# Kernel tuning notes

Hardware: AMD Instinct MI355X
Metric: run time of the kernel (lower is better)

Reference implementation:

```python
import jax, jax.numpy as jnp
import numpy as np

B, D, NT, NZ = 16384, 64, 128, 2048


def setup_inputs() -> dict:
    key = jax.random.key(0)
    ks = jax.random.split(key, 5)
    return {
        "t": jax.random.uniform(ks[0], (1,), dtype=jnp.float32),
        "z": jax.random.normal(ks[1], (B, D), dtype=jnp.float32),
        "logp_z": jnp.zeros((B, 1), jnp.float32),
        "centres_z": jax.random.normal(ks[2], (NZ, D), dtype=jnp.float32),
        "log_sigmas_z": jnp.zeros((NZ,), jnp.float32),
        "centres_t": jax.random.normal(ks[3], (NT, 1), dtype=jnp.float32),
        "log_sigmas_t": jnp.zeros((NT,), jnp.float32),
        "W": 0.01 * jax.random.normal(ks[4], (D, NT, NZ + 1), dtype=jnp.float32),
    }


def _gauss(r):
    return jnp.exp(-r * r)


def _forward(t, z, centres_z, log_sigmas_z, centres_t, log_sigmas_t, W):
    # time RBF features Phi_t: (NT,)
    r_t = jnp.abs(t.reshape(1, 1) - centres_t.reshape(1, -1)) / jnp.exp(log_sigmas_t)
    phi_t = _gauss(r_t).reshape(-1)
    W_t = jnp.einsum('dij,i->dj', W, phi_t)  # (D, NZ+1)
    Wz, bias = W_t[:, :-1], W_t[:, -1]       # bias comes from the appended ones column
    # z RBF features via squared-distance identity (avoids [B,NZ,D] blowup)
    sq = (jnp.sum(z * z, axis=1, keepdims=True)
          + jnp.sum(centres_z * centres_z, axis=1)[None, :]
          - 2.0 * z @ centres_z.T)
    sq = jnp.maximum(sq, 0.0)                 # (B, NZ) squared distances
    inv_s2 = jnp.exp(-2.0 * log_sigmas_z)     # 1/sigma_j^2, (NZ,)
    phi_z = jnp.exp(-sq * inv_s2)             # gaussian(||z-c_j||/s_j), (B, NZ)
    dz_dt = phi_z @ Wz.T + bias               # (B, D)
    # exact Jacobian trace for gaussian basis:
    #   d phi_j / d z_i = -2 * phi_j * (z_i - c_{j,i}) / s_j^2
    #   tr(J)_b = sum_j phi_{b,j} * inv_s2_j * (-2) * (sum_i Wz[i,j] z_{b,i} - sum_i Wz[i,j] c_{j,i})
    q = jnp.einsum('dj,jd->j', Wz, centres_z)  # (NZ,)
    trace = -2.0 * jnp.sum(phi_z * inv_s2 * (z @ Wz - q), axis=1)  # (B,)
    dlogp_z_dt = -trace[:, None]               # (B, 1)
    return dz_dt, dlogp_z_dt


def reference(t, z, logp_z, centres_z, log_sigmas_z, centres_t, log_sigmas_t, W):
    return _forward(t, z, centres_z, log_sigmas_z, centres_t, log_sigmas_t, W)
```

## Files before the change

kernel.cpp:

```cpp
#include <hip/hip_runtime.h>
#include <math.h>

typedef unsigned int uint;
typedef unsigned short ushort;
typedef unsigned char uchar;
typedef unsigned long ulong_;
typedef __attribute__((ext_vector_type(4))) float f32x4;

#define BB  16384
#define DD  64
#define NT_ 128
#define NZ_ 2048
#define NJ_ 2049

#define BIAS_OFF 0
#define IL2_OFF  64
#define A0_OFF   2112
#define NIQ_OFF  4160
#define CZ8A_OFF 6208
#define CZ8B_OFF 22592
#define WZ8A_OFF 38976
#define WZ8B_OFF 55360
#define WZBP_OFF 71744
#define PART_OFF 104512

#if __has_builtin(__builtin_amdgcn_cvt_pk_fp8_f32)
__device__ __forceinline__ uint pk4_fp8(float a, float b, float c, float d) {
  int v = __builtin_amdgcn_cvt_pk_fp8_f32(a, b, 0, false);
  v = __builtin_amdgcn_cvt_pk_fp8_f32(c, d, v, true);
  return (uint)v;
}
__device__ __forceinline__ uchar f8_1(float x) {
  return (uchar)(__builtin_amdgcn_cvt_pk_fp8_f32(x, x, 0, false) & 0xFF);
}
#else
__device__ __forceinline__ uint sw_f8(float x) {
  uint u = __float_as_uint(x);
  uint s = (u >> 24) & 0x80u;
  float ax = __uint_as_float(u & 0x7FFFFFFFu);
  if (!(ax >= 0.015625f)) return s;
  if (ax >= 448.f) return s | 0x7Eu;
  uint q = __float_as_uint(ax);
  q += 0x7FFFFu + ((q >> 20) & 1u);
  uint e = (q >> 23) - 120u;
  return s | ((e & 0xFu) << 3) | ((q >> 20) & 7u);
}
__device__ __forceinline__ uchar f8_1(float x) { return (uchar)sw_f8(x); }
__device__ __forceinline__ uint pk4_fp8(float a, float b, float c, float d) {
  return sw_f8(a) | (sw_f8(b) << 8) | (sw_f8(c) << 16) | (sw_f8(d) << 24);
}
#endif

__global__ __launch_bounds__(256) void k_wt1(
    const float* __restrict__ t, const float* __restrict__ ct,
    const float* __restrict__ lst, const float* __restrict__ W,
    float* __restrict__ part)
{
  __shared__ float ph[32];
  int tx = threadIdx.x;
  int d  = blockIdx.y;
  int ic = blockIdx.z;
  if (tx < 32) {
    int i = ic * 32 + tx;
    float r = fabsf(t[0] - ct[i]) * __expf(-lst[i]);
    ph[tx] = __expf(-r * r);
  }
  __syncthreads();
  int j = blockIdx.x * 256 + tx;
  if (j >= NJ_) return;
  const float* Wp = W + (size_t)d * NT_ * NJ_ + (size_t)(ic * 32) * NJ_ + j;
  float acc = 0.f;
#pragma unroll
  for (int k = 0; k < 32; ++k) acc += Wp[(size_t)k * NJ_] * ph[k];
  part[((size_t)ic * 64 + d) * NJ_ + j] = acc;
}

__global__ __launch_bounds__(256) void k_prep2(
    const float* __restrict__ part, const float* __restrict__ cz,
    const float* __restrict__ lsz,
    float* __restrict__ bias,
    float* __restrict__ il2a, float* __restrict__ a0a, float* __restrict__ niqa,
    uchar* __restrict__ cz8a, uchar* __restrict__ cz8b,
    uchar* __restrict__ wz8a, uchar* __restrict__ wz8b,
    uchar* __restrict__ wzbp8)
{
  __shared__ float wt[64][9];
  int tid = threadIdx.x;
  int cb0 = blockIdx.x * 8;
#pragma unroll
  for (int h = 0; h < 2; ++h) {
    int f = h * 256 + tid;
    int d = f >> 3, c = f & 7;
    size_t idx = (size_t)d * NJ_ + cb0 + c;
    float s = part[idx] + part[(size_t)64 * NJ_ + idx]
            + part[(size_t)128 * NJ_ + idx] + part[(size_t)192 * NJ_ + idx];
    wt[d][c] = s;
    int cg = cb0 + c;
    wzbp8[((size_t)(cg >> 5) * 64 + d) * 32 + (cg & 31)] = f8_1(s);
  }
  if (blockIdx.x == 0 && tid < 64) {
    size_t idx = (size_t)tid * NJ_ + 2048;
    bias[tid] = part[idx] + part[(size_t)64 * NJ_ + idx]
              + part[(size_t)128 * NJ_ + idx] + part[(size_t)192 * NJ_ + idx];
  }
  __syncthreads();
  int cl = tid >> 5;
  int k  = tid & 31;
  int c  = cb0 + cl;
  float cv0 = cz[(size_t)c * DD + k];
  float cv1 = cz[(size_t)c * DD + 32 + k];
  cz8a[(size_t)c * 32 + k] = f8_1(cv0);
  cz8b[(size_t)c * 32 + k] = f8_1(cv1);
  float w0 = wt[k][cl], w1 = wt[32 + k][cl];
  wz8a[(size_t)c * 32 + k] = f8_1(w0);
  wz8b[(size_t)c * 32 + k] = f8_1(w1);
  float ca = cv0 * cv0 + cv1 * cv1;
  float qa = w0 * cv0 + w1 * cv1;
  qa += __shfl_xor(qa, 1);  ca += __shfl_xor(ca, 1);
  qa += __shfl_xor(qa, 2);  ca += __shfl_xor(ca, 2);
  qa += __shfl_xor(qa, 4);  ca += __shfl_xor(ca, 4);
  qa += __shfl_xor(qa, 8);  ca += __shfl_xor(ca, 8);
  qa += __shfl_xor(qa, 16); ca += __shfl_xor(ca, 16);
  if (k == 0) {
    float inv = __expf(-2.f * lsz[c]);
    float il2 = inv * 1.44269504f;
    il2a[c] = il2;
    a0a[c]  = -ca * il2;
    niqa[c] = -inv * qa;
  }
}

__global__ __launch_bounds__(256, 2) void k_fused(
    const float* __restrict__ z,
    const uchar* __restrict__ cz8a, const uchar* __restrict__ cz8b,
    const uchar* __restrict__ wz8a, const uchar* __restrict__ wz8b,
    const uchar* __restrict__ wzbp8,
    const float* __restrict__ il2a, const float* __restrict__ a0a,
    const float* __restrict__ niqa,
    const float* __restrict__ bias, float* __restrict__ out)
{
  __shared__ float eps[32 * 68];
  __shared__ float dlr[4][32];

  int tid  = threadIdx.x;
  int ws   = tid >> 6;
  int lane = tid & 63;
  int lrow = lane & 15, quad = lane >> 4;
  int b0 = blockIdx.x * 32;

  long az[2][2];
  float nzz[2];
#pragma unroll
  for (int mt = 0; mt < 2; ++mt) {
    const float* zr = z + (size_t)(b0 + mt * 16 + lrow) * DD + quad * 8;
    float4 v0 = *(const float4*)zr;
    float4 v1 = *(const float4*)(zr + 4);
    float4 v2 = *(const float4*)(zr + 32);
    float4 v3 = *(const float4*)(zr + 36);
    uint l0 = pk4_fp8(v0.x, v0.y, v0.z, v0.w);
    uint l1 = pk4_fp8(v1.x, v1.y, v1.z, v1.w);
    uint h0 = pk4_fp8(v2.x, v2.y, v2.z, v2.w);
    uint h1 = pk4_fp8(v3.x, v3.y, v3.z, v3.w);
    az[mt][0] = (long)(((ulong_)l1 << 32) | l0);
    az[mt][1] = (long)(((ulong_)h1 << 32) | h0);
    float ss = v0.x * v0.x + v0.y * v0.y + v0.z * v0.z + v0.w * v0.w
             + v1.x * v1.x + v1.y * v1.y + v1.z * v1.z + v1.w * v1.w
             + v2.x * v2.x + v2.y * v2.y + v2.z * v2.z + v2.w * v2.w
             + v3.x * v3.x + v3.y * v3.y + v3.z * v3.z + v3.w * v3.w;
    ss += __shfl_xor(ss, 16);
    ss += __shfl_xor(ss, 32);
    nzz[mt] = -ss;
  }

  f32x4 acc[2][4];
#pragma unroll
  for (int mt = 0; mt < 2; ++mt)
#pragma unroll
    for (int nt = 0; nt < 4; ++nt) acc[mt][nt] = (f32x4){0.f, 0.f, 0.f, 0.f};
  float dl[2] = {0.f, 0.f};

  const f32x4 zero = (f32x4){0.f, 0.f, 0.f, 0.f};
  int cbase = ws * 512;

  long Abc0[2][2], Abc1[2][2], Abw0[2][2], Abw1[2][2], Abb[2][4];
#define LOADB(PAR, C0)                                                         \
  do {                                                                         \
    int c0_ = (C0);                                                            \
    _Pragma("unroll")                                                          \
    for (int nt = 0; nt < 2; ++nt) {                                           \
      int cg_ = c0_ + nt * 16 + lrow;                                          \
      size_t ro_ = (size_t)cg_ * 32 + quad * 8;                                \
      Abc0[PAR][nt] = *(const long*)(cz8a + ro_);                              \
      Abc1[PAR][nt] = *(const long*)(cz8b + ro_);                              \
      Abw0[PAR][nt] = *(const long*)(wz8a + ro_);                              \
      Abw1[PAR][nt] = *(const long*)(wz8b + ro_);                              \
    }                                                                          \
    size_t cb_ = (size_t)(c0_ >> 5) * 64 * 32;                                 \
    _Pragma("unroll")                                                          \
    for (int nt = 0; nt < 4; ++nt)                                             \
      Abb[PAR][nt] =                                                           \
          *(const long*)(wzbp8 + cb_ + (size_t)(nt * 16 + lrow) * 32 + quad * 8); \
  } while (0)

  LOADB(0, cbase);
#pragma unroll 2
  for (int it = 0; it < 16; ++it) {
    int par = it & 1;
    int c0  = cbase + it * 32;

    float4 ilv[2], a0v[2], nqv[2];
#pragma unroll
    for (int nt = 0; nt < 2; ++nt) {
      int cb = c0 + nt * 16 + quad * 4;
      ilv[nt] = *(const float4*)&il2a[cb];
      a0v[nt] = *(const float4*)&a0a[cb];
      nqv[nt] = *(const float4*)&niqa[cb];
    }

    f32x4 d1a[2][2], d2a[2][2];
#pragma unroll
    for (int nt = 0; nt < 2; ++nt)
#pragma unroll
      for (int mt = 0; mt < 2; ++mt) {
        f32x4 d1 = __builtin_amdgcn_mfma_f32_16x16x32_fp8_fp8(Abc0[par][nt], az[mt][0], zero, 0, 0, 0);
        d1       = __builtin_amdgcn_mfma_f32_16x16x32_fp8_fp8(Abc1[par][nt], az[mt][1], d1,   0, 0, 0);
        f32x4 d2 = __builtin_amdgcn_mfma_f32_16x16x32_fp8_fp8(Abw0[par][nt], az[mt][0], zero, 0, 0, 0);
        d2       = __builtin_amdgcn_mfma_f32_16x16x32_fp8_fp8(Abw1[par][nt], az[mt][1], d2,   0, 0, 0);
        d1a[nt][mt] = d1;
        d2a[nt][mt] = d2;
      }

    LOADB(par ^ 1, cbase + ((it + 1) & 15) * 32);

    uint u00, u01, u10, u11;
#pragma unroll
    for (int mt = 0; mt < 2; ++mt)
#pragma unroll
      for (int nt = 0; nt < 2; ++nt) {
        float pv[4];
#pragma unroll
        for (int i = 0; i < 4; ++i) {
          float il2 = ilv[nt][i];
          float t2  = d1a[nt][mt][i] + d1a[nt][mt][i];
          float uu  = fmaf(il2, nzz[mt], a0v[nt][i]);
          float e   = fmaf(t2, il2, uu);
          e = fminf(e, 0.f);
          float p;
          asm("v_exp_f32 %0, %1" : "=v"(p) : "v"(e));
          float g = fmaf(d2a[nt][mt][i] * 0.69314718f, il2, nqv[nt][i]);
          dl[mt] = fmaf(p, g, dl[mt]);
          pv[i] = p;
        }
        uint uv = pk4_fp8(pv[0], pv[1], pv[2], pv[3]);
        if (mt == 0) { if (nt == 0) u00 = uv; else u01 = uv; }
        else         { if (nt == 0) u10 = uv; else u11 = uv; }
      }

    int  sl = lrow + ((lane & 16) << 1);
    bool hh = lane >= 32;
    uint l0a = __shfl(u00, sl),      l1a = __shfl(u01, sl);
    uint h0a = __shfl(u00, sl + 16), h1a = __shfl(u01, sl + 16);
    uint lo0 = hh ? l1a : l0a,       hi0 = hh ? h1a : h0a;
    long ap0 = (long)(((ulong_)hi0 << 32) | lo0);
    uint l0b = __shfl(u10, sl),      l1b = __shfl(u11, sl);
    uint h0b = __shfl(u10, sl + 16), h1b = __shfl(u11, sl + 16);
    uint lo1 = hh ? l1b : l0b,       hi1 = hh ? h1b : h0b;
    long ap1 = (long)(((ulong_)hi1 << 32) | lo1);

    __builtin_amdgcn_s_setprio(1);
#pragma unroll
    for (int nt = 0; nt < 4; ++nt) {
      acc[0][nt] = __builtin_amdgcn_mfma_f32_16x16x32_fp8_fp8(ap0, Abb[par][nt], acc[0][nt], 0, 0, 0);
      acc[1][nt] = __builtin_amdgcn_mfma_f32_16x16x32_fp8_fp8(ap1, Abb[par][nt], acc[1][nt], 0, 0, 0);
    }
    __builtin_amdgcn_s_setprio(0);
  }
#undef LOADB

#pragma unroll
  for (int mt = 0; mt < 2; ++mt) {
    float v = dl[mt];
    v += __shfl_xor(v, 16);
    v += __shfl_xor(v, 32);
    if (quad == 0) dlr[ws][mt * 16 + lrow] = v;
  }

  for (int s = 0; s < 4; ++s) {
    __syncthreads();
    if (ws == s) {
#pragma unroll
      for (int mt = 0; mt < 2; ++mt)
#pragma unroll
        for (int nt = 0; nt < 4; ++nt)
#pragma unroll
          for (int i = 0; i < 4; ++i) {
            int r = mt * 16 + quad * 4 + i;
            int d = nt * 16 + lrow;
            if (s == 0) eps[r * 68 + d] = acc[mt][nt][i];
            else        eps[r * 68 + d] += acc[mt][nt][i];
          }
    }
  }
  __syncthreads();

  {
    int r = tid >> 3, d0 = (tid & 7) * 8;
    float4 e0 = *(const float4*)&eps[r * 68 + d0];
    float4 e1 = *(const float4*)&eps[r * 68 + d0 + 4];
    float4 bv0 = *(const float4*)&bias[d0];
    float4 bv1 = *(const float4*)&bias[d0 + 4];
    float4 o0, o1;
    o0.x = e0.x + bv0.x; o0.y = e0.y + bv0.y; o0.z = e0.z + bv0.z; o0.w = e0.w + bv0.w;
    o1.x = e1.x + bv1.x; o1.y = e1.y + bv1.y; o1.z = e1.z + bv1.z; o1.w = e1.w + bv1.w;
    *(float4*)&out[(size_t)(b0 + r) * DD + d0]     = o0;
    *(float4*)&out[(size_t)(b0 + r) * DD + d0 + 4] = o1;
  }
  if (tid < 32) {
    float s = dlr[0][tid] + dlr[1][tid] + dlr[2][tid] + dlr[3][tid];
    out[(size_t)BB * DD + b0 + tid] = 2.f * s;
  }
}

extern "C" void kernel_launch(void* const* d_in, const int* in_sizes, int n_in,
                              void* d_out, int out_size, void* d_ws, size_t ws_size,
                              hipStream_t stream)
{
  const float* t   = (const float*)d_in[0];
  const float* z   = (const float*)d_in[1];
  const float* cz  = (const float*)d_in[3];
  const float* lsz = (const float*)d_in[4];
  const float* ct  = (const float*)d_in[5];
  const float* lst = (const float*)d_in[6];
  const float* W   = (const float*)d_in[7];
  float* out = (float*)d_out;
  float* ws  = (float*)d_ws;

  float*  bias = ws + BIAS_OFF;
  float*  il2a = ws + IL2_OFF;
  float*  a0a  = ws + A0_OFF;
  float*  niqa = ws + NIQ_OFF;
  uchar*  cz8a = (uchar*)(ws + CZ8A_OFF);
  uchar*  cz8b = (uchar*)(ws + CZ8B_OFF);
  uchar*  wz8a = (uchar*)(ws + WZ8A_OFF);
  uchar*  wz8b = (uchar*)(ws + WZ8B_OFF);
  uchar*  wzbp8 = (uchar*)(ws + WZBP_OFF);
  float*  part = ws + PART_OFF;

  k_wt1<<<dim3(9, 64, 4), 256, 0, stream>>>(t, ct, lst, W, part);
  k_prep2<<<dim3(256), 256, 0, stream>>>(part, cz, lsz, bias,
                                         il2a, a0a, niqa,
                                         cz8a, cz8b, wz8a, wz8b, wzbp8);
  k_fused<<<dim3(BB / 32), 256, 0, stream>>>(z, cz8a, cz8b,
                                             wz8a, wz8b, wzbp8,
                                             il2a, a0a, niqa, bias, out);
}
```

Baseline: 137.5 us.

## Shrink fused kernel row tile to 16 and drop register double-buffering

The fused kernel now handles 16 batch rows per block instead of 32, doubling the grid. It also removes the software-pipelined double-buffered B-operand loads in favour of plain per-iteration loads with no unrolling, and drops the launch-bounds occupancy hint. This lowers register pressure and raises parallelism. The cost is that every centre/weight fragment is loaded twice as often per batch row, which halves operand reuse, and load latency is no longer hidden by prefetch.

```diff
diff --git a/kernel.cpp b/kernel.cpp
--- a/kernel.cpp
+++ b/kernel.cpp
@@ -130,7 +130,7 @@
   }
 }
 
-__global__ __launch_bounds__(256, 2) void k_fused(
+__global__ __launch_bounds__(256) void k_fused(
     const float* __restrict__ z,
     const uchar* __restrict__ cz8a, const uchar* __restrict__ cz8b,
     const uchar* __restrict__ wz8a, const uchar* __restrict__ wz8b,
@@ -139,20 +139,19 @@
     const float* __restrict__ niqa,
     const float* __restrict__ bias, float* __restrict__ out)
 {
-  __shared__ float eps[32 * 68];
-  __shared__ float dlr[4][32];
+  __shared__ float eps[16 * 68];
+  __shared__ float dlr[4][16];
 
   int tid  = threadIdx.x;
   int ws   = tid >> 6;
   int lane = tid & 63;
   int lrow = lane & 15, quad = lane >> 4;
-  int b0 = blockIdx.x * 32;
-
-  long az[2][2];
-  float nzz[2];
-#pragma unroll
-  for (int mt = 0; mt < 2; ++mt) {
-    const float* zr = z + (size_t)(b0 + mt * 16 + lrow) * DD + quad * 8;
+  int b0 = blockIdx.x * 16;
+
+  long az[2];
+  float nzz;
+  {
+    const float* zr = z + (size_t)(b0 + lrow) * DD + quad * 8;
     float4 v0 = *(const float4*)zr;
     float4 v1 = *(const float4*)(zr + 4);
     float4 v2 = *(const float4*)(zr + 32);
@@ -161,161 +160,129 @@
     uint l1 = pk4_fp8(v1.x, v1.y, v1.z, v1.w);
     uint h0 = pk4_fp8(v2.x, v2.y, v2.z, v2.w);
     uint h1 = pk4_fp8(v3.x, v3.y, v3.z, v3.w);
-    az[mt][0] = (long)(((ulong_)l1 << 32) | l0);
-    az[mt][1] = (long)(((ulong_)h1 << 32) | h0);
+    az[0] = (long)(((ulong_)l1 << 32) | l0);
+    az[1] = (long)(((ulong_)h1 << 32) | h0);
     float ss = v0.x * v0.x + v0.y * v0.y + v0.z * v0.z + v0.w * v0.w
              + v1.x * v1.x + v1.y * v1.y + v1.z * v1.z + v1.w * v1.w
              + v2.x * v2.x + v2.y * v2.y + v2.z * v2.z + v2.w * v2.w
              + v3.x * v3.x + v3.y * v3.y + v3.z * v3.z + v3.w * v3.w;
     ss += __shfl_xor(ss, 16);
     ss += __shfl_xor(ss, 32);
-    nzz[mt] = -ss;
-  }
-
-  f32x4 acc[2][4];
-#pragma unroll
-  for (int mt = 0; mt < 2; ++mt)
-#pragma unroll
-    for (int nt = 0; nt < 4; ++nt) acc[mt][nt] = (f32x4){0.f, 0.f, 0.f, 0.f};
-  float dl[2] = {0.f, 0.f};
+    nzz = -ss;
+  }
+
+  f32x4 acc[4];
+#pragma unroll
+  for (int nt = 0; nt < 4; ++nt) acc[nt] = (f32x4){0.f, 0.f, 0.f, 0.f};
+  float dl = 0.f;
 
   const f32x4 zero = (f32x4){0.f, 0.f, 0.f, 0.f};
   int cbase = ws * 512;
 
-  long Abc0[2][2], Abc1[2][2], Abw0[2][2], Abw1[2][2], Abb[2][4];
-#define LOADB(PAR, C0)                                                         \
-  do {                                                                         \
-    int c0_ = (C0);                                                            \
-    _Pragma("unroll")                                                          \
-    for (int nt = 0; nt < 2; ++nt) {                                           \
-      int cg_ = c0_ + nt * 16 + lrow;                                          \
-      size_t ro_ = (size_t)cg_ * 32 + quad * 8;                                \
-      Abc0[PAR][nt] = *(const long*)(cz8a + ro_);                              \
-      Abc1[PAR][nt] = *(const long*)(cz8b + ro_);                              \
-      Abw0[PAR][nt] = *(const long*)(wz8a + ro_);                              \
-      Abw1[PAR][nt] = *(const long*)(wz8b + ro_);                              \
-    }                                                                          \
-    size_t cb_ = (size_t)(c0_ >> 5) * 64 * 32;                                 \
-    _Pragma("unroll")                                                          \
-    for (int nt = 0; nt < 4; ++nt)                                             \
-      Abb[PAR][nt] =                                                           \
-          *(const long*)(wzbp8 + cb_ + (size_t)(nt * 16 + lrow) * 32 + quad * 8); \
-  } while (0)
-
-  LOADB(0, cbase);
-#pragma unroll 2
+#pragma unroll 1
   for (int it = 0; it < 16; ++it) {
-    int par = it & 1;
-    int c0  = cbase + it * 32;
-
+    int c0 = cbase + it * 32;
+
+    long Abc0[2], Abc1[2], Abw0[2], Abw1[2], Abb[4];
     float4 ilv[2], a0v[2], nqv[2];
 #pragma unroll
     for (int nt = 0; nt < 2; ++nt) {
+      int cg = c0 + nt * 16 + lrow;
+      size_t ro = (size_t)cg * 32 + quad * 8;
+      Abc0[nt] = *(const long*)(cz8a + ro);
+      Abc1[nt] = *(const long*)(cz8b + ro);
+      Abw0[nt] = *(const long*)(wz8a + ro);
+      Abw1[nt] = *(const long*)(wz8b + ro);
       int cb = c0 + nt * 16 + quad * 4;
       ilv[nt] = *(const float4*)&il2a[cb];
       a0v[nt] = *(const float4*)&a0a[cb];
       nqv[nt] = *(const float4*)&niqa[cb];
     }
-
-    f32x4 d1a[2][2], d2a[2][2];
-#pragma unroll
-    for (int nt = 0; nt < 2; ++nt)
-#pragma unroll
-      for (int mt = 0; mt < 2; ++mt) {
-        f32x4 d1 = __builtin_amdgcn_mfma_f32_16x16x32_fp8_fp8(Abc0[par][nt], az[mt][0], zero, 0, 0, 0);
-        d1       = __builtin_amdgcn_mfma_f32_16x16x32_fp8_fp8(Abc1[par][nt], az[mt][1], d1,   0, 0, 0);
-        f32x4 d2 = __builtin_amdgcn_mfma_f32_16x16x32_fp8_fp8(Abw0[par][nt], az[mt][0], zero, 0, 0, 0);
-        d2       = __builtin_amdgcn_mfma_f32_16x16x32_fp8_fp8(Abw1[par][nt], az[mt][1], d2,   0, 0, 0);
-        d1a[nt][mt] = d1;
-        d2a[nt][mt] = d2;
+    {
+      size_t cb_ = (size_t)(c0 >> 5) * 64 * 32;
+#pragma unroll
+      for (int nt = 0; nt < 4; ++nt)
+        Abb[nt] = *(const long*)(wzbp8 + cb_ + (size_t)(nt * 16 + lrow) * 32 + quad * 8);
+    }
+
+    f32x4 d1a[2], d2a[2];
+#pragma unroll
+    for (int nt = 0; nt < 2; ++nt) {
+      f32x4 d1 = __builtin_amdgcn_mfma_f32_16x16x32_fp8_fp8(Abc0[nt], az[0], zero, 0, 0, 0);
+      d1       = __builtin_amdgcn_mfma_f32_16x16x32_fp8_fp8(Abc1[nt], az[1], d1,   0, 0, 0);
+      f32x4 d2 = __builtin_amdgcn_mfma_f32_16x16x32_fp8_fp8(Abw0[nt], az[0], zero, 0, 0, 0);
+      d2       = __builtin_amdgcn_mfma_f32_16x16x32_fp8_fp8(Abw1[nt], az[1], d2,   0, 0, 0);
+      d1a[nt] = d1;
+      d2a[nt] = d2;
+    }
+
+    uint u0, u1;
+#pragma unroll
+    for (int nt = 0; nt < 2; ++nt) {
+      float pv[4];
+#pragma unroll
+      for (int i = 0; i < 4; ++i) {
+        float il2 = ilv[nt][i];
+        float t2  = d1a[nt][i] + d1a[nt][i];
+        float uu  = fmaf(il2, nzz, a0v[nt][i]);
+        float e   = fmaf(t2, il2, uu);
+        e = fminf(e, 0.f);
+        float p;
+        asm("v_exp_f32 %0, %1" : "=v"(p) : "v"(e));
+        float g = fmaf(d2a[nt][i] * 0.69314718f, il2, nqv[nt][i]);
+        dl = fmaf(p, g, dl);
+        pv[i] = p;
       }
-
-    LOADB(par ^ 1, cbase + ((it + 1) & 15) * 32);
-
-    uint u00, u01, u10, u11;
-#pragma unroll
-    for (int mt = 0; mt < 2; ++mt)
-#pragma unroll
-      for (int nt = 0; nt < 2; ++nt) {
-        float pv[4];
-#pragma unroll
-        for (int i = 0; i < 4; ++i) {
-          float il2 = ilv[nt][i];
-          float t2  = d1a[nt][mt][i] + d1a[nt][mt][i];
-          float uu  = fmaf(il2, nzz[mt], a0v[nt][i]);
-          float e   = fmaf(t2, il2, uu);
-          e = fminf(e, 0.f);
-          float p;
-          asm("v_exp_f32 %0, %1" : "=v"(p) : "v"(e));
-          float g = fmaf(d2a[nt][mt][i] * 0.69314718f, il2, nqv[nt][i]);
-          dl[mt] = fmaf(p, g, dl[mt]);
-          pv[i] = p;
-        }
-        uint uv = pk4_fp8(pv[0], pv[1], pv[2], pv[3]);
-        if (mt == 0) { if (nt == 0) u00 = uv; else u01 = uv; }
-        else         { if (nt == 0) u10 = uv; else u11 = uv; }
-      }
+      uint uv = pk4_fp8(pv[0], pv[1], pv[2], pv[3]);
+      if (nt == 0) u0 = uv; else u1 = uv;
+    }
 
     int  sl = lrow + ((lane & 16) << 1);
     bool hh = lane >= 32;
-    uint l0a = __shfl(u00, sl),      l1a = __shfl(u01, sl);
-    uint h0a = __shfl(u00, sl + 16), h1a = __shfl(u01, sl + 16);
-    uint lo0 = hh ? l1a : l0a,       hi0 = hh ? h1a : h0a;
+    uint l0a = __shfl(u0, sl),      l1a = __shfl(u1, sl);
+    uint h0a = __shfl(u0, sl + 16), h1a = __shfl(u1, sl + 16);
+    uint lo0 = hh ? l1a : l0a,      hi0 = hh ? h1a : h0a;
     long ap0 = (long)(((ulong_)hi0 << 32) | lo0);
-    uint l0b = __shfl(u10, sl),      l1b = __shfl(u11, sl);
-    uint h0b = __shfl(u10, sl + 16), h1b = __shfl(u11, sl + 16);
-    uint lo1 = hh ? l1b : l0b,       hi1 = hh ? h1b : h0b;
-    long ap1 = (long)(((ulong_)hi1 << 32) | lo1);
 
     __builtin_amdgcn_s_setprio(1);
 #pragma unroll
-    for (int nt = 0; nt < 4; ++nt) {
-      acc[0][nt] = __builtin_amdgcn_mfma_f32_16x16x32_fp8_fp8(ap0, Abb[par][nt], acc[0][nt], 0, 0, 0);
-      acc[1][nt] = __builtin_amdgcn_mfma_f32_16x16x32_fp8_fp8(ap1, Abb[par][nt], acc[1][nt], 0, 0, 0);
-    }
+    for (int nt = 0; nt < 4; ++nt)
+      acc[nt] = __builtin_amdgcn_mfma_f32_16x16x32_fp8_fp8(ap0, Abb[nt], acc[nt], 0, 0, 0);
     __builtin_amdgcn_s_setprio(0);
   }
-#undef LOADB
-
-#pragma unroll
-  for (int mt = 0; mt < 2; ++mt) {
-    float v = dl[mt];
+
+  {
+    float v = dl;
     v += __shfl_xor(v, 16);
     v += __shfl_xor(v, 32);
-    if (quad == 0) dlr[ws][mt * 16 + lrow] = v;
+    if (quad == 0) dlr[ws][lrow] = v;
   }
 
   for (int s = 0; s < 4; ++s) {
     __syncthreads();
     if (ws == s) {
 #pragma unroll
-      for (int mt = 0; mt < 2; ++mt)
-#pragma unroll
-        for (int nt = 0; nt < 4; ++nt)
-#pragma unroll
-          for (int i = 0; i < 4; ++i) {
-            int r = mt * 16 + quad * 4 + i;
-            int d = nt * 16 + lrow;
-            if (s == 0) eps[r * 68 + d] = acc[mt][nt][i];
-            else        eps[r * 68 + d] += acc[mt][nt][i];
-          }
+      for (int nt = 0; nt < 4; ++nt)
+#pragma unroll
+        for (int i = 0; i < 4; ++i) {
+          int r = quad * 4 + i;
+          int d = nt * 16 + lrow;
+          if (s == 0) eps[r * 68 + d] = acc[nt][i];
+          else        eps[r * 68 + d] += acc[nt][i];
+        }
     }
   }
   __syncthreads();
 
   {
-    int r = tid >> 3, d0 = (tid & 7) * 8;
+    int r = tid >> 4, d0 = (tid & 15) * 4;
     float4 e0 = *(const float4*)&eps[r * 68 + d0];
-    float4 e1 = *(const float4*)&eps[r * 68 + d0 + 4];
     float4 bv0 = *(const float4*)&bias[d0];
-    float4 bv1 = *(const float4*)&bias[d0 + 4];
-    float4 o0, o1;
+    float4 o0;
     o0.x = e0.x + bv0.x; o0.y = e0.y + bv0.y; o0.z = e0.z + bv0.z; o0.w = e0.w + bv0.w;
-    o1.x = e1.x + bv1.x; o1.y = e1.y + bv1.y; o1.z = e1.z + bv1.z; o1.w = e1.w + bv1.w;
-    *(float4*)&out[(size_t)(b0 + r) * DD + d0]     = o0;
-    *(float4*)&out[(size_t)(b0 + r) * DD + d0 + 4] = o1;
-  }
-  if (tid < 32) {
+    *(float4*)&out[(size_t)(b0 + r) * DD + d0] = o0;
+  }
+  if (tid < 16) {
     float s = dlr[0][tid] + dlr[1][tid] + dlr[2][tid] + dlr[3][tid];
     out[(size_t)BB * DD + b0 + tid] = 2.f * s;
   }
@@ -350,7 +317,7 @@
   k_prep2<<<dim3(256), 256, 0, stream>>>(part, cz, lsz, bias,
                                          il2a, a0a, niqa,
                                          cz8a, cz8b, wz8a, wz8b, wzbp8);
-  k_fused<<<dim3(BB / 32), 256, 0, stream>>>(z, cz8a, cz8b,
+  k_fused<<<dim3(BB / 16), 256, 0, stream>>>(z, cz8a, cz8b,
                                              wz8a, wz8b, wzbp8,
                                              il2a, a0a, niqa, bias, out);
 }
```

Measured after the change: 153.0 us. +11.2%, slower.

## Stage per-tile B operands into LDS via global_load_lds double buffering

Applied to the files above, without the earlier changes.

Replaces the per-lane register prefetch of fp8 centre/weight tiles and per-centre constants with asynchronous global-to-LDS loads into a per-wave double buffer, waited on with vmcnt. Each iteration reads its operands from LDS, which cuts register pressure and the scattered small global loads. It also precomputes inv sigma^2 so the exponent and trace terms need fewer FMAs. The cost is more LDS use per block (about 57KB), which may limit occupancy. Correctness relies on the manual waitcnt ordering, since there is no barrier between the async LDS writes and the reads.

```diff
diff --git a/kernel.cpp b/kernel.cpp
--- a/kernel.cpp
+++ b/kernel.cpp
@@ -17,12 +17,13 @@
 #define IL2_OFF  64
 #define A0_OFF   2112
 #define NIQ_OFF  4160
-#define CZ8A_OFF 6208
-#define CZ8B_OFF 22592
-#define WZ8A_OFF 38976
-#define WZ8B_OFF 55360
-#define WZBP_OFF 71744
-#define PART_OFF 104512
+#define INV_OFF  6208
+#define CZ8A_OFF 8256
+#define CZ8B_OFF 24640
+#define WZ8A_OFF 41024
+#define WZ8B_OFF 57408
+#define WZBP_OFF 73792
+#define PART_OFF 106560
 
 #if __has_builtin(__builtin_amdgcn_cvt_pk_fp8_f32)
 __device__ __forceinline__ uint pk4_fp8(float a, float b, float c, float d) {
@@ -50,6 +51,12 @@
   return sw_f8(a) | (sw_f8(b) << 8) | (sw_f8(c) << 16) | (sw_f8(d) << 24);
 }
 #endif
+
+__device__ __forceinline__ void stage16(const void* g, void* l) {
+  __builtin_amdgcn_global_load_lds(
+      (const __attribute__((address_space(1))) uint*)g,
+      (__attribute__((address_space(3))) uint*)l, 16, 0, 0);
+}
 
 __global__ __launch_bounds__(256) void k_wt1(
     const float* __restrict__ t, const float* __restrict__ ct,
@@ -80,6 +87,7 @@
     const float* __restrict__ lsz,
     float* __restrict__ bias,
     float* __restrict__ il2a, float* __restrict__ a0a, float* __restrict__ niqa,
+    float* __restrict__ inva,
     uchar* __restrict__ cz8a, uchar* __restrict__ cz8b,
     uchar* __restrict__ wz8a, uchar* __restrict__ wz8b,
     uchar* __restrict__ wzbp8)
@@ -127,6 +135,7 @@
     il2a[c] = il2;
     a0a[c]  = -ca * il2;
     niqa[c] = -inv * qa;
+    inva[c] = inv;
   }
 }
 
@@ -136,11 +145,12 @@
     const uchar* __restrict__ wz8a, const uchar* __restrict__ wz8b,
     const uchar* __restrict__ wzbp8,
     const float* __restrict__ il2a, const float* __restrict__ a0a,
-    const float* __restrict__ niqa,
+    const float* __restrict__ niqa, const float* __restrict__ inva,
     const float* __restrict__ bias, float* __restrict__ out)
 {
-  __shared__ float eps[32 * 68];
+  __shared__ __align__(16) uchar smem[4 * 2 * 7168];
   __shared__ float dlr[4][32];
+  float* eps = (float*)smem;
 
   int tid  = threadIdx.x;
   int ws   = tid >> 6;
@@ -172,6 +182,10 @@
     nzz[mt] = -ss;
   }
 
+  int asel = (lane >> 3) & 3;
+  const float* myA = asel == 0 ? il2a : asel == 1 ? a0a : asel == 2 ? niqa : inva;
+  const uchar* myAb = (const uchar*)myA + (size_t)(lane & 7) * 16;
+
   f32x4 acc[2][4];
 #pragma unroll
   for (int mt = 0; mt < 2; ++mt)
@@ -181,57 +195,63 @@
 
   const f32x4 zero = (f32x4){0.f, 0.f, 0.f, 0.f};
   int cbase = ws * 512;
-
-  long Abc0[2][2], Abc1[2][2], Abw0[2][2], Abw1[2][2], Abb[2][4];
-#define LOADB(PAR, C0)                                                         \
+  uchar* wlds = smem + (size_t)ws * 14336;
+
+#define STAGE(B, C0)                                                           \
   do {                                                                         \
-    int c0_ = (C0);                                                            \
-    _Pragma("unroll")                                                          \
-    for (int nt = 0; nt < 2; ++nt) {                                           \
-      int cg_ = c0_ + nt * 16 + lrow;                                          \
-      size_t ro_ = (size_t)cg_ * 32 + quad * 8;                                \
-      Abc0[PAR][nt] = *(const long*)(cz8a + ro_);                              \
-      Abc1[PAR][nt] = *(const long*)(cz8b + ro_);                              \
-      Abw0[PAR][nt] = *(const long*)(wz8a + ro_);                              \
-      Abw1[PAR][nt] = *(const long*)(wz8b + ro_);                              \
-    }                                                                          \
-    size_t cb_ = (size_t)(c0_ >> 5) * 64 * 32;                                 \
-    _Pragma("unroll")                                                          \
-    for (int nt = 0; nt < 4; ++nt)                                             \
-      Abb[PAR][nt] =                                                           \
-          *(const long*)(wzbp8 + cb_ + (size_t)(nt * 16 + lrow) * 32 + quad * 8); \
+    uchar* lb_ = wlds + (B) * 7168;                                            \
+    size_t go_ = (size_t)(C0) * 32 + (size_t)lane * 16;                        \
+    stage16(cz8a + go_, lb_);                                                  \
+    stage16(cz8b + go_, lb_ + 1024);                                           \
+    stage16(wz8a + go_, lb_ + 2048);                                           \
+    stage16(wz8b + go_, lb_ + 3072);                                           \
+    const uchar* wb_ = wzbp8 + ((size_t)((C0) >> 5)) * 2048 + (size_t)lane * 16; \
+    stage16(wb_, lb_ + 4096);                                                  \
+    stage16(wb_ + 1024, lb_ + 5120);                                           \
+    stage16(myAb + (size_t)(C0) * 4, lb_ + 6144);                              \
   } while (0)
 
-  LOADB(0, cbase);
+  STAGE(0, cbase);
 #pragma unroll 2
   for (int it = 0; it < 16; ++it) {
-    int par = it & 1;
-    int c0  = cbase + it * 32;
-
-    float4 ilv[2], a0v[2], nqv[2];
+    int buf = it & 1;
+    STAGE(buf ^ 1, cbase + ((it + 1) & 15) * 32);
+    asm volatile("s_waitcnt vmcnt(7)" ::: "memory");
+    __builtin_amdgcn_sched_barrier(0);
+
+    const uchar* tb = wlds + buf * 7168;
+    long Abc0[2], Abc1[2], Abw0[2], Abw1[2], Abb[4];
+    float4 ilv[2], a0v[2], nqv[2], ivv[2];
 #pragma unroll
     for (int nt = 0; nt < 2; ++nt) {
-      int cb = c0 + nt * 16 + quad * 4;
-      ilv[nt] = *(const float4*)&il2a[cb];
-      a0v[nt] = *(const float4*)&a0a[cb];
-      nqv[nt] = *(const float4*)&niqa[cb];
+      int off = (nt * 16 + lrow) * 32 + quad * 8;
+      Abc0[nt] = *(const long*)(tb + off);
+      Abc1[nt] = *(const long*)(tb + 1024 + off);
+      Abw0[nt] = *(const long*)(tb + 2048 + off);
+      Abw1[nt] = *(const long*)(tb + 3072 + off);
+      int coff = (nt * 16 + quad * 4) * 4;
+      ilv[nt] = *(const float4*)(tb + 6144 + coff);
+      a0v[nt] = *(const float4*)(tb + 6144 + 128 + coff);
+      nqv[nt] = *(const float4*)(tb + 6144 + 256 + coff);
+      ivv[nt] = *(const float4*)(tb + 6144 + 384 + coff);
     }
+#pragma unroll
+    for (int nt = 0; nt < 4; ++nt)
+      Abb[nt] = *(const long*)(tb + 4096 + (nt * 16 + lrow) * 32 + quad * 8);
 
     f32x4 d1a[2][2], d2a[2][2];
 #pragma unroll
     for (int nt = 0; nt < 2; ++nt)
 #pragma unroll
       for (int mt = 0; mt < 2; ++mt) {
-        f32x4 d1 = __builtin_amdgcn_mfma_f32_16x16x32_fp8_fp8(Abc0[par][nt], az[mt][0], zero, 0, 0, 0);
-        d1       = __builtin_amdgcn_mfma_f32_16x16x32_fp8_fp8(Abc1[par][nt], az[mt][1], d1,   0, 0, 0);
-        f32x4 d2 = __builtin_amdgcn_mfma_f32_16x16x32_fp8_fp8(Abw0[par][nt], az[mt][0], zero, 0, 0, 0);
-        d2       = __builtin_amdgcn_mfma_f32_16x16x32_fp8_fp8(Abw1[par][nt], az[mt][1], d2,   0, 0, 0);
+        f32x4 d1 = __builtin_amdgcn_mfma_f32_16x16x32_fp8_fp8(Abc0[nt], az[mt][0], zero, 0, 0, 0);
+        d1       = __builtin_amdgcn_mfma_f32_16x16x32_fp8_fp8(Abc1[nt], az[mt][1], d1,   0, 0, 0);
+        f32x4 d2 = __builtin_amdgcn_mfma_f32_16x16x32_fp8_fp8(Abw0[nt], az[mt][0], zero, 0, 0, 0);
+        d2       = __builtin_amdgcn_mfma_f32_16x16x32_fp8_fp8(Abw1[nt], az[mt][1], d2,   0, 0, 0);
         d1a[nt][mt] = d1;
         d2a[nt][mt] = d2;
       }
 
-    LOADB(par ^ 1, cbase + ((it + 1) & 15) * 32);
-
     uint u00, u01, u10, u11;
 #pragma unroll
     for (int mt = 0; mt < 2; ++mt)
@@ -240,14 +260,12 @@
         float pv[4];
 #pragma unroll
         for (int i = 0; i < 4; ++i) {
-          float il2 = ilv[nt][i];
-          float t2  = d1a[nt][mt][i] + d1a[nt][mt][i];
-          float uu  = fmaf(il2, nzz[mt], a0v[nt][i]);
-          float e   = fmaf(t2, il2, uu);
+          float tt = fmaf(d1a[nt][mt][i], 2.f, nzz[mt]);
+          float e  = fmaf(ilv[nt][i], tt, a0v[nt][i]);
           e = fminf(e, 0.f);
           float p;
           asm("v_exp_f32 %0, %1" : "=v"(p) : "v"(e));
-          float g = fmaf(d2a[nt][mt][i] * 0.69314718f, il2, nqv[nt][i]);
+          float g = fmaf(d2a[nt][mt][i], ivv[nt][i], nqv[nt][i]);
           dl[mt] = fmaf(p, g, dl[mt]);
           pv[i] = p;
         }
@@ -270,12 +288,13 @@
     __builtin_amdgcn_s_setprio(1);
 #pragma unroll
     for (int nt = 0; nt < 4; ++nt) {
-      acc[0][nt] = __builtin_amdgcn_mfma_f32_16x16x32_fp8_fp8(ap0, Abb[par][nt], acc[0][nt], 0, 0, 0);
-      acc[1][nt] = __builtin_amdgcn_mfma_f32_16x16x32_fp8_fp8(ap1, Abb[par][nt], acc[1][nt], 0, 0, 0);
+      acc[0][nt] = __builtin_amdgcn_mfma_f32_16x16x32_fp8_fp8(ap0, Abb[nt], acc[0][nt], 0, 0, 0);
+      acc[1][nt] = __builtin_amdgcn_mfma_f32_16x16x32_fp8_fp8(ap1, Abb[nt], acc[1][nt], 0, 0, 0);
     }
     __builtin_amdgcn_s_setprio(0);
   }
-#undef LOADB
+#undef STAGE
+  asm volatile("s_waitcnt vmcnt(0)" ::: "memory");
 
 #pragma unroll
   for (int mt = 0; mt < 2; ++mt) {
@@ -339,6 +358,7 @@
   float*  il2a = ws + IL2_OFF;
   float*  a0a  = ws + A0_OFF;
   float*  niqa = ws + NIQ_OFF;
+  float*  inva = ws + INV_OFF;
   uchar*  cz8a = (uchar*)(ws + CZ8A_OFF);
   uchar*  cz8b = (uchar*)(ws + CZ8B_OFF);
   uchar*  wz8a = (uchar*)(ws + WZ8A_OFF);
@@ -348,9 +368,9 @@
 
   k_wt1<<<dim3(9, 64, 4), 256, 0, stream>>>(t, ct, lst, W, part);
   k_prep2<<<dim3(256), 256, 0, stream>>>(part, cz, lsz, bias,
-                                         il2a, a0a, niqa,
+                                         il2a, a0a, niqa, inva,
                                          cz8a, cz8b, wz8a, wz8b, wzbp8);
   k_fused<<<dim3(BB / 32), 256, 0, stream>>>(z, cz8a, cz8b,
                                              wz8a, wz8b, wzbp8,
-                                             il2a, a0a, niqa, bias, out);
-}
+                                             il2a, a0a, niqa, inva, bias, out);
+}
```

Result: slower. 143.2 us (+4.1%).
